# Optimization experiments

Measured on AMD Instinct MI355X. Metric: run time of the kernel, lower is better.

## Reference

```python
import jax, jax.numpy as jnp
import numpy as np

RADIUS = 0.2
NSAMPLE = 32
USE_XYZ = True


def setup_inputs() -> dict:
    key = jax.random.key(0)
    k1, k2, k3 = jax.random.split(key, 3)
    B, N, S, C = 8, 16384, 1024, 64
    xyz = jax.random.uniform(k1, (B, N, 3), dtype=jnp.float32)
    new_xyz = jax.random.uniform(k2, (B, S, 3), dtype=jnp.float32)
    features = jax.random.normal(k3, (B, C, N), dtype=jnp.float32)
    return {"xyz": xyz, "new_xyz": new_xyz, "features": features}


def _ball_query(xyz, new_xyz, radius, nsample):
    """For each query point, the first `nsample` point indices within `radius`,
    padded with the first valid index (0 if none) — matches the CUDA kernel."""
    B, N, _ = xyz.shape
    # squared distances [B, S, N]
    d2 = jnp.sum((new_xyz[:, :, None, :] - xyz[:, None, :, :]) ** 2, axis=-1)
    within = d2 < (radius * radius)
    # encode: valid points keep their index, invalid get sentinel N; sorting
    # then yields the first-in-order valid indices, as the CUDA kernel does.
    keys = jnp.where(within, jnp.arange(N, dtype=jnp.int32)[None, None, :], N)
    idx = jnp.sort(keys, axis=-1)[:, :, :nsample]          # [B, S, K]
    first = idx[:, :, 0:1]
    first = jnp.where(first < N, first, 0)                 # no neighbor -> 0
    idx = jnp.where(idx < N, idx, first)
    return idx.astype(jnp.int32)


def reference(xyz, new_xyz, features):
    idx = _ball_query(xyz, new_xyz, RADIUS, NSAMPLE)       # [B, S, K] int32
    # group xyz: gather [B, S, K, 3] then center on new_xyz
    grouped_xyz = jnp.take_along_axis(xyz[:, None, :, :], idx[:, :, :, None], axis=2)
    grouped_xyz = grouped_xyz - new_xyz[:, :, None, :]
    grouped_xyz = jnp.transpose(grouped_xyz, (0, 3, 1, 2))  # [B, 3, S, K]
    # group features: [B, C, 1, N] gathered with [B, 1, S, K] -> [B, C, S, K]
    grouped_feats = jnp.take_along_axis(features[:, :, :, None].transpose(0, 1, 3, 2),
                                        idx[:, None, :, :], axis=3)
    if USE_XYZ:
        return jnp.concatenate([grouped_xyz, grouped_feats], axis=1)  # [B, 3+C, S, K]
    return grouped_feats
```

## Files before the change

### kernel.cpp

```cpp
#include <hip/hip_runtime.h>


#define BB 8
#define NN 16384
#define SS 1024
#define CC 64
#define NSAMP 32
#define OUTCH (3 + CC)

#define R2 0.04f

__global__ __launch_bounds__(256) void query_kernel(
    const float* __restrict__ xyz,
    const float* __restrict__ new_xyz,
    int* __restrict__ idxq,
    float* __restrict__ out)
{
    __shared__ int sidx[4][NSAMP];

    const int t    = threadIdx.x;
    const int wave = t >> 6;
    const int lane = t & 63;
    const int q    = blockIdx.x * 4 + wave;
    const int b    = q >> 10;
    const int s    = q & (SS - 1);

    const float* xb = xyz + (size_t)b * NN * 3;
    const float qx = new_xyz[((size_t)b * SS + s) * 3 + 0];
    const float qy = new_xyz[((size_t)b * SS + s) * 3 + 1];
    const float qz = new_xyz[((size_t)b * SS + s) * 3 + 2];
    const unsigned long long below = (1ull << lane) - 1ull;

    int count = 0;
    for (int base = 0; base < NN; base += 512) {
        float d2[8];
        #pragma unroll
        for (int j = 0; j < 8; ++j) {
            const int i = base + j * 64 + lane;
            const float dx = qx - xb[i * 3 + 0];
            const float dy = qy - xb[i * 3 + 1];
            const float dz = qz - xb[i * 3 + 2];
            d2[j] = __fadd_rn(__fadd_rn(__fmul_rn(dx, dx),
                                        __fmul_rn(dy, dy)),
                              __fmul_rn(dz, dz));
        }
        #pragma unroll
        for (int j = 0; j < 8; ++j) {
            const bool within = d2[j] < R2;
            const unsigned long long m = __ballot(within);
            if (within) {
                const int pos = count + __popcll(m & below);
                if (pos < NSAMP) sidx[wave][pos] = base + j * 64 + lane;
            }
            count += __popcll(m);
        }
        if (count >= NSAMP) break;
    }
    __syncthreads();
    const int cnt = count < NSAMP ? count : NSAMP;
    const int first = (cnt > 0) ? sidx[wave][0] : 0;
    if (lane < NSAMP && lane >= cnt) sidx[wave][lane] = first;
    __syncthreads();

    if (lane < NSAMP) {
        const int k = lane;
        const int idx = sidx[wave][k];
        idxq[(size_t)q * NSAMP + k] = idx;
        const float gx = xb[idx * 3 + 0] - qx;
        const float gy = xb[idx * 3 + 1] - qy;
        const float gz = xb[idx * 3 + 2] - qz;
        const size_t o = (((size_t)b * OUTCH + 0) * SS + s) * NSAMP + k;
        out[o + 0 * (size_t)SS * NSAMP] = gx;
        out[o + 1 * (size_t)SS * NSAMP] = gy;
        out[o + 2 * (size_t)SS * NSAMP] = gz;
    }
}

__global__ __launch_bounds__(512) void gather_kernel(
    const float* __restrict__ feats,
    const int*   __restrict__ idxq,
    float* __restrict__ out)
{
    __shared__ float row[NN];

    const int c = blockIdx.x;
    const int b = blockIdx.y;
    const int t = threadIdx.x;

    const float* fr = feats + ((size_t)b * CC + c) * NN;
    #pragma unroll
    for (int i = 0; i < 8; ++i) {
        const int o = (i * 512 + t) * 4;
        *(float4*)(row + o) = *(const float4*)(fr + o);
    }
    __syncthreads();

    const int k4 = (t & 7) * 4;
    const int s0 = t >> 3;
    const int*  ib = idxq + (size_t)b * SS * NSAMP;
    float* ob = out + (((size_t)b * OUTCH + 3 + c) * SS) * NSAMP;
    #pragma unroll
    for (int it = 0; it < 16; ++it) {
        const int s = it * 64 + s0;
        const int4 id = *(const int4*)(ib + (size_t)s * NSAMP + k4);
        float4 v;
        v.x = row[id.x];
        v.y = row[id.y];
        v.z = row[id.z];
        v.w = row[id.w];
        *(float4*)(ob + (size_t)s * NSAMP + k4) = v;
    }
}

__global__ __launch_bounds__(64) void qg_fused(
    const float* __restrict__ xyz, const float* __restrict__ new_xyz,
    const float* __restrict__ feats, float* __restrict__ out)
{
    const int bs   = blockIdx.x;
    const int b    = bs >> 10;
    const int s    = bs & (SS - 1);
    const int lane = threadIdx.x;

    const float* xb = xyz + (size_t)b * NN * 3;
    const float qx = new_xyz[((size_t)b * SS + s) * 3 + 0];
    const float qy = new_xyz[((size_t)b * SS + s) * 3 + 1];
    const float qz = new_xyz[((size_t)b * SS + s) * 3 + 2];

    __shared__ int sidx[NSAMP];
    int count = 0;
    for (int base = 0; base < NN; base += 64) {
        const int i = base + lane;
        const float dx = qx - xb[i * 3 + 0];
        const float dy = qy - xb[i * 3 + 1];
        const float dz = qz - xb[i * 3 + 2];
        const float d2 = __fadd_rn(__fadd_rn(__fmul_rn(dx, dx),
                                             __fmul_rn(dy, dy)),
                                   __fmul_rn(dz, dz));
        const bool within = d2 < R2;
        const unsigned long long m = __ballot(within);
        if (within) {
            const int pos = count + __popcll(m & ((1ull << lane) - 1ull));
            if (pos < NSAMP) sidx[pos] = i;
        }
        count += __popcll(m);
        if (count >= NSAMP) break;
    }
    __syncthreads();
    const int cnt = count < NSAMP ? count : NSAMP;
    const int first = (cnt > 0) ? sidx[0] : 0;
    if (lane < NSAMP && lane >= cnt) sidx[lane] = first;
    __syncthreads();

    const int k    = lane & 31;
    const int half = lane >> 5;
    const int idx  = sidx[k];
    const size_t obase = (((size_t)b * OUTCH + 0) * SS + s) * NSAMP + k;
    if (half == 0) {
        out[obase + 0 * (size_t)SS * NSAMP] = xb[idx * 3 + 0] - qx;
        out[obase + 1 * (size_t)SS * NSAMP] = xb[idx * 3 + 1] - qy;
        out[obase + 2 * (size_t)SS * NSAMP] = xb[idx * 3 + 2] - qz;
    }
    const float* fb = feats + (size_t)b * CC * NN;
    const size_t fo = (((size_t)b * OUTCH + 3) * SS + s) * NSAMP + k;
    for (int cch = half; cch < CC; cch += 2) {
        out[fo + (size_t)cch * SS * NSAMP] = fb[(size_t)cch * NN + idx];
    }
}

extern "C" void kernel_launch(void* const* d_in, const int* in_sizes, int n_in,
                              void* d_out, int out_size, void* d_ws, size_t ws_size,
                              hipStream_t stream) {
    const float* xyz     = (const float*)d_in[0];
    const float* new_xyz = (const float*)d_in[1];
    const float* feats   = (const float*)d_in[2];
    float* out           = (float*)d_out;

    const size_t idx_bytes = (size_t)BB * SS * NSAMP * sizeof(int);

    if (ws_size >= idx_bytes) {
        int* idxq = (int*)d_ws;
        query_kernel<<<2048, 256, 0, stream>>>(xyz, new_xyz, idxq, out);
        gather_kernel<<<dim3(CC, BB), 512, 0, stream>>>(feats, idxq, out);
    } else {
        qg_fused<<<BB * SS, 64, 0, stream>>>(xyz, new_xyz, feats, out);
    }
}
```

Measured before the change: 115.0 us.

## Fuse ball query and feature gather into one cooperative kernel with grid sync

Replaces the two-kernel query/gather sequence with a single cooperative kernel of 512 blocks. Each block first loads its feature row into shared memory, then runs ball queries for two query points per wave, writing indices straight to global memory, and after a grid-wide sync performs the gather. The intent is to remove the second launch and hide the feature-row load behind the query phase. In exchange the whole grid must be co-resident, query parallelism drops to 512 blocks of 8 waves, and padding now goes through global memory instead of shared memory. If the cooperative launch fails, it falls back to the old two-kernel path.

```diff
diff --git a/kernel.cpp b/kernel.cpp
--- a/kernel.cpp
+++ b/kernel.cpp
@@ -1,4 +1,7 @@
 #include <hip/hip_runtime.h>
+#include <hip/hip_cooperative_groups.h>
+
+namespace cg = cooperative_groups;
 
 
 #define BB 8
@@ -10,11 +13,106 @@
 
 #define R2 0.04f
 
-__global__ __launch_bounds__(256) void query_kernel(
+__global__ __launch_bounds__(512, 4) void fused_kernel(
     const float* __restrict__ xyz,
     const float* __restrict__ new_xyz,
+    const float* __restrict__ feats,
     int* __restrict__ idxq,
     float* __restrict__ out)
+{
+    __shared__ float row[NN];
+
+    const int blk  = blockIdx.x;
+    const int c    = blk & 63;
+    const int b    = blk >> 6;
+    const int t    = threadIdx.x;
+    const int wave = t >> 6;
+    const int lane = t & 63;
+
+    const float* fr = feats + ((size_t)b * CC + c) * NN;
+    #pragma unroll
+    for (int i = 0; i < 8; ++i) {
+        const int o = (i * 512 + t) * 4;
+        *(float4*)(row + o) = *(const float4*)(fr + o);
+    }
+
+    const float* xb = xyz + (size_t)b * NN * 3;
+    const unsigned long long below = (1ull << lane) - 1ull;
+
+    #pragma unroll
+    for (int qi = 0; qi < 2; ++qi) {
+        const int s = ((blk & 63) << 3) + wave + qi * 512;
+        const int q = (b << 10) + s;
+        const float qx = new_xyz[((size_t)b * SS + s) * 3 + 0];
+        const float qy = new_xyz[((size_t)b * SS + s) * 3 + 1];
+        const float qz = new_xyz[((size_t)b * SS + s) * 3 + 2];
+
+        int count = 0;
+        for (int base = 0; base < NN; base += 512) {
+            float d2[8];
+            #pragma unroll
+            for (int j = 0; j < 8; ++j) {
+                const int i = base + j * 64 + lane;
+                const float dx = qx - xb[i * 3 + 0];
+                const float dy = qy - xb[i * 3 + 1];
+                const float dz = qz - xb[i * 3 + 2];
+                d2[j] = __fadd_rn(__fadd_rn(__fmul_rn(dx, dx),
+                                            __fmul_rn(dy, dy)),
+                                  __fmul_rn(dz, dz));
+            }
+            #pragma unroll
+            for (int j = 0; j < 8; ++j) {
+                const bool within = d2[j] < R2;
+                const unsigned long long m = __ballot(within);
+                if (within) {
+                    const int pos = count + __popcll(m & below);
+                    if (pos < NSAMP)
+                        idxq[(size_t)q * NSAMP + pos] = base + j * 64 + lane;
+                }
+                count += __popcll(m);
+            }
+            if (count >= NSAMP) break;
+        }
+
+        __builtin_amdgcn_s_waitcnt(0);
+        if (lane < NSAMP) {
+            const int cnt = count < NSAMP ? count : NSAMP;
+            int idx = 0;
+            if (cnt > 0) idx = idxq[(size_t)q * NSAMP + (lane < cnt ? lane : 0)];
+            if (lane >= cnt) idxq[(size_t)q * NSAMP + lane] = idx;
+            const float gx = xb[idx * 3 + 0] - qx;
+            const float gy = xb[idx * 3 + 1] - qy;
+            const float gz = xb[idx * 3 + 2] - qz;
+            const size_t o = (((size_t)b * OUTCH + 0) * SS + s) * NSAMP + lane;
+            out[o + 0 * (size_t)SS * NSAMP] = gx;
+            out[o + 1 * (size_t)SS * NSAMP] = gy;
+            out[o + 2 * (size_t)SS * NSAMP] = gz;
+        }
+    }
+
+    __threadfence();
+    cg::this_grid().sync();
+
+    const int k4 = (t & 7) * 4;
+    const int s0 = t >> 3;
+    const int* ib = idxq + (size_t)b * SS * NSAMP;
+    float* ob = out + (((size_t)b * OUTCH + 3 + c) * SS) * NSAMP;
+    #pragma unroll
+    for (int it = 0; it < 16; ++it) {
+        const int s = it * 64 + s0;
+        const int4 id = *(const int4*)(ib + (size_t)s * NSAMP + k4);
+        float4 v;
+        v.x = row[id.x];
+        v.y = row[id.y];
+        v.z = row[id.z];
+        v.w = row[id.w];
+        *(float4*)(ob + (size_t)s * NSAMP + k4) = v;
+    }
+}
+
+__global__ __launch_bounds__(256) void query_kernel(
+    const float* __restrict__ xyz, const float* __restrict__ new_xyz,
+    int* __restrict__ idxq, float* __restrict__ out)
 {
     __shared__ int sidx[4][NSAMP];
 
@@ -63,13 +161,12 @@
     __syncthreads();
 
     if (lane < NSAMP) {
-        const int k = lane;
-        const int idx = sidx[wave][k];
-        idxq[(size_t)q * NSAMP + k] = idx;
+        const int idx = sidx[wave][lane];
+        idxq[(size_t)q * NSAMP + lane] = idx;
         const float gx = xb[idx * 3 + 0] - qx;
         const float gy = xb[idx * 3 + 1] - qy;
         const float gz = xb[idx * 3 + 2] - qz;
-        const size_t o = (((size_t)b * OUTCH + 0) * SS + s) * NSAMP + k;
+        const size_t o = (((size_t)b * OUTCH + 0) * SS + s) * NSAMP + lane;
         out[o + 0 * (size_t)SS * NSAMP] = gx;
         out[o + 1 * (size_t)SS * NSAMP] = gy;
         out[o + 2 * (size_t)SS * NSAMP] = gz;
@@ -77,8 +174,7 @@
 }
 
 __global__ __launch_bounds__(512) void gather_kernel(
-    const float* __restrict__ feats,
-    const int*   __restrict__ idxq,
+    const float* __restrict__ feats, const int* __restrict__ idxq,
     float* __restrict__ out)
 {
     __shared__ float row[NN];
@@ -97,7 +193,7 @@
 
     const int k4 = (t & 7) * 4;
     const int s0 = t >> 3;
-    const int*  ib = idxq + (size_t)b * SS * NSAMP;
+    const int* ib = idxq + (size_t)b * SS * NSAMP;
     float* ob = out + (((size_t)b * OUTCH + 3 + c) * SS) * NSAMP;
     #pragma unroll
     for (int it = 0; it < 16; ++it) {
@@ -179,8 +275,15 @@
 
     if (ws_size >= idx_bytes) {
         int* idxq = (int*)d_ws;
-        query_kernel<<<2048, 256, 0, stream>>>(xyz, new_xyz, idxq, out);
-        gather_kernel<<<dim3(CC, BB), 512, 0, stream>>>(feats, idxq, out);
+        void* args[] = {(void*)&xyz, (void*)&new_xyz, (void*)&feats,
+                        (void*)&idxq, (void*)&out};
+        hipError_t err = hipLaunchCooperativeKernel(
+            (const void*)fused_kernel, dim3(512), dim3(512), args, 0, stream);
+        if (err != hipSuccess) {
+            (void)hipGetLastError();
+            query_kernel<<<2048, 256, 0, stream>>>(xyz, new_xyz, idxq, out);
+            gather_kernel<<<dim3(CC, BB), 512, 0, stream>>>(feats, idxq, out);
+        }
     } else {
         qg_fused<<<BB * SS, 64, 0, stream>>>(xyz, new_xyz, feats, out);
     }
```

After: 283.3 us. +146.3%, slower.
